# Optimization experiments

Hardware: AMD Instinct MI355X
Metric: run time of the kernel (lower is better)

The kernel has to match this reference:

```python
import jax, jax.numpy as jnp
import numpy as np

B = 32            # batch size
N = 100           # n_nodes (== MAX_N_NODES here)
MAXN = 100        # MAX_N_NODES
H = 256           # HIDDEN_DIM_FEATURES_EXTRACTOR
HA = 1024         # HIDDEN_DIM_ACTOR
HC = 512          # HIDDEN_DIM_CRITIC
K_ACTIVE = 5000   # exact number of active mask entries per batch element


def setup_inputs() -> dict:
    key = jax.random.key(0)
    ks = jax.random.split(key, 16)
    feat = jax.random.normal(ks[0], (B, N + 1, H), jnp.float32)
    # mask: exactly K_ACTIVE ones among N*N per batch row (dim == K for all rows)
    rng = np.random.default_rng(0)
    mask = np.zeros((B, N * N), np.float32)
    for i in range(B):
        mask[i, rng.choice(N * N, size=K_ACTIVE, replace=False)] = 1.0
    mask = jnp.asarray(mask).reshape(B, N, N)
    ext_mask = jnp.concatenate([jnp.zeros((B, 1, N), jnp.float32), mask], axis=1)  # [B, N+1, N]
    embedded_features = jnp.concatenate([feat, ext_mask], axis=2)  # [B, N+1, H+N]

    def lin(k, fi, fo):
        s = 1.0 / np.sqrt(fi)
        return (jax.random.uniform(k, (fi, fo), jnp.float32, -s, s),
                jax.random.uniform(jax.random.fold_in(k, 1), (fo,), jnp.float32, -s, s))

    aW1, ab1 = lin(ks[1], 3 * H, HA)
    aW2, ab2 = lin(ks[2], HA, HA)
    aW3, ab3 = lin(ks[3], HA, 1)
    cW1, cb1 = lin(ks[4], H, HC)
    cW2, cb2 = lin(ks[5], HC, HC)
    cW3, cb3 = lin(ks[6], HC, 1)
    return dict(embedded_features=embedded_features,
                aW1=aW1, ab1=ab1, aW2=aW2, ab2=ab2, aW3=aW3, ab3=ab3,
                cW1=cW1, cb1=cb1, cW2=cW2, cb2=cb2, cW3=cW3, cb3=cb3,
                K=K_ACTIVE)


def reference(embedded_features, aW1, ab1, aW2, ab2, aW3, ab3,
              cW1, cb1, cW2, cb2, cW3, cb3, K):
    # decompose features
    gn = embedded_features[:, :, :H]
    ext_mask = embedded_features[:, :, H:]
    g = gn[:, :1, :]                      # [B,1,H] graph embedding
    nodes = gn[:, 1:, :]                  # [B,N,H] node embeddings
    mask = ext_mask[:, 1:, :].reshape(B, -1)  # [B, N*N]

    # indexes of active pairs (stable top_k -> ascending indices among ones, like nonzero)
    _, idx = jax.lax.top_k(mask, K)       # [B,K] int32
    idx1 = idx // N
    idx2 = idx % N
    n1 = jnp.take_along_axis(nodes, idx1[:, :, None], axis=1)  # [B,K,H]
    n2 = jnp.take_along_axis(nodes, idx2[:, :, None], axis=1)  # [B,K,H]
    pairs = jnp.concatenate([jnp.broadcast_to(g, (B, K, H)), n1, n2], axis=-1)  # [B,K,3H]

    # actor MLP (tanh hidden activations)
    h = jnp.tanh(pairs @ aW1 + ab1)
    h = jnp.tanh(h @ aW2 + ab2)
    logits = h @ aW3 + ab3                # [B,K,1]
    pi = jax.nn.softmax(logits, axis=1)   # softmax over the K gathered pairs

    # scatter back into padded grid
    shaped = jnp.zeros((B, N * N), pi.dtype).at[jnp.arange(B)[:, None], idx].set(pi[..., 0])
    filled = jnp.zeros((B, MAXN, MAXN), pi.dtype).at[:, :N, :N].set(shaped.reshape(B, N, N))
    filled = filled.reshape(B, MAXN * MAXN)

    # critic MLP on graph embedding
    hv = jnp.tanh(g @ cW1 + cb1)
    hv = jnp.tanh(hv @ cW2 + cb2)
    value = hv @ cW3 + cb3                # [B,1,1]
    return filled, value
```

## Files before the change

kernel.cpp:

```cpp
#include <hip/hip_runtime.h>
#include <stdint.h>

#define AS1 __attribute__((address_space(1)))
#define AS3 __attribute__((address_space(3)))

typedef __bf16 bf16x8 __attribute__((ext_vector_type(8)));
typedef float  f32x4  __attribute__((ext_vector_type(4)));
typedef int    i32x8  __attribute__((ext_vector_type(8)));
typedef float  f32x16 __attribute__((ext_vector_type(16)));

__device__ __forceinline__ float tanh_fast(float x){
    float e = __expf(2.0f * x);
    return 1.0f - 2.0f * __builtin_amdgcn_rcpf(e + 1.0f);
}

__device__ __forceinline__ unsigned short f2bf(float f){
    unsigned int u = __float_as_uint(f);
    u = (u + 0x7fffu + ((u >> 16) & 1u)) >> 16;
    return (unsigned short)u;
}

#define B2F(u, lo, hi) { lo = __uint_as_float((u) << 16); hi = __uint_as_float((u) & 0xffff0000u); }

__global__ __launch_bounds__(256) void k_prep(
    const float* __restrict__ ef,  const float* __restrict__ aW1, const float* __restrict__ ab1,
    const float* __restrict__ aW2,
    const float* __restrict__ cW1, const float* __restrict__ cb1,
    const float* __restrict__ cW2, const float* __restrict__ cb2,
    const float* __restrict__ cW3, const float* __restrict__ cb3,
    int* __restrict__ pairs, unsigned short* __restrict__ w1t,
    unsigned char* __restrict__ w2b, float* __restrict__ g1o, float* __restrict__ out,
    int* __restrict__ qctr)
{
    int blk = blockIdx.x;
    int t = threadIdx.x;
    __shared__ int s_base, s_woff[4], s_wc[4];
    __shared__ float gs[256];
    __shared__ float h1[512], h2[512], wred[4];

    if (blk == 0 && t == 0) qctr[0] = 0;

    if (blk < 32){
        int b = blk;
        if (t == 0) s_base = 0;
        __syncthreads();
        int lane = t & 63, w = t >> 6;
        for (int ch = 0; ch < 40; ++ch){
            int pos = ch * 256 + t;
            bool valid = false;
            if (pos < 10000){
                int r = pos / 100, c = pos - (pos / 100) * 100;
                valid = ef[(size_t)b * 35956 + (size_t)(1 + r) * 356 + 256 + c] != 0.0f;
            }
            unsigned long long bal = __ballot(valid);
            if (lane == 0) s_wc[w] = __popcll(bal);
            __syncthreads();
            if (t == 0){
                int r = s_base;
                for (int q = 0; q < 4; ++q){ s_woff[q] = r; r += s_wc[q]; }
                s_base = r;
            }
            __syncthreads();
            if (valid){
                int rank = __popcll(bal & ((1ull << lane) - 1ull));
                int o = s_woff[w] + rank;
                if (o < 5000) pairs[b * 5000 + o] = pos;
            }
            __syncthreads();
        }
    } else if (blk < 288){
        int tid = (blk - 32) * 256 + t;
        int k8 = tid & 31, c = (tid >> 5) & 1023, s = tid >> 15;
        const float* src = aW1 + (size_t)(256 + s * 256 + k8 * 8) * 1024 + c;
        unsigned int* dst = (unsigned int*)(w1t + (size_t)tid * 8);
#pragma unroll
        for (int jj = 0; jj < 4; ++jj){
            unsigned short lo = f2bf(src[(size_t)(2 * jj) * 1024]);
            unsigned short hi = f2bf(src[(size_t)(2 * jj + 1) * 1024]);
            dst[jj] = (unsigned int)lo | ((unsigned int)hi << 16);
        }
    } else if (blk < 416){
        int tid = (blk - 288) * 256 + t;
        int lane = tid & 63, kt = (tid >> 6) & 15, ct = tid >> 10;
        int lh = lane >> 5, n = lane & 31;
        const float* src = aW2 + (size_t)(kt * 64 + lh * 32) * 1024 + ct * 32 + n;
        unsigned int d[4] = {0u, 0u, 0u, 0u};
#pragma unroll
        for (int j = 0; j < 32; ++j){
            float a = src[(size_t)j * 1024] * 128.0f;
            float f = fabsf(a);
            unsigned int m = f < 0.25f ? 0u : f < 0.75f ? 1u : f < 1.25f ? 2u :
                             f < 1.75f ? 3u : f < 2.5f  ? 4u : f < 3.5f  ? 5u :
                             f < 5.0f  ? 6u : 7u;
            unsigned int nib = m | (a < 0.0f ? 8u : 0u);
            d[j >> 3] |= nib << (4 * (j & 7));
        }
        *(uint4*)(w2b + (size_t)(ct * 16 + kt) * 1024 + lane * 16) =
            make_uint4(d[0], d[1], d[2], d[3]);
    } else if (blk < 448){
        int b = blk - 416;
        gs[t] = ef[(size_t)b * 35956 + t];
        __syncthreads();
        float a0 = 0.f, a1 = 0.f, a2 = 0.f, a3 = 0.f;
        for (int i = 0; i < 256; ++i){
            float gi = gs[i];
            const float* row = aW1 + (size_t)i * 1024;
            a0 += gi * row[t];       a1 += gi * row[t + 256];
            a2 += gi * row[t + 512]; a3 += gi * row[t + 768];
        }
        float* o = g1o + (size_t)b * 1024;
        o[t] = a0 + ab1[t];             o[t + 256] = a1 + ab1[t + 256];
        o[t + 512] = a2 + ab1[t + 512]; o[t + 768] = a3 + ab1[t + 768];
    } else {
        int b = blk - 448;
        gs[t] = ef[(size_t)b * 35956 + t];
        __syncthreads();
        for (int o = t; o < 512; o += 256){
            float a = cb1[o];
            for (int i = 0; i < 256; ++i) a += gs[i] * cW1[(size_t)i * 512 + o];
            h1[o] = tanh_fast(a);
        }
        __syncthreads();
        for (int o = t; o < 512; o += 256){
            float a = cb2[o];
            for (int i = 0; i < 512; ++i) a += h1[i] * cW2[(size_t)i * 512 + o];
            h2[o] = tanh_fast(a);
        }
        __syncthreads();
        float p = h2[t] * cW3[t] + h2[t + 256] * cW3[t + 256];
        for (int m = 32; m >= 1; m >>= 1) p += __shfl_xor(p, m);
        if ((t & 63) == 0) wred[t >> 6] = p;
        __syncthreads();
        if (t == 0) out[320000 + b] = wred[0] + wred[1] + wred[2] + wred[3] + cb3[0];
    }
}

__global__ __launch_bounds__(256) void k_p(const float* __restrict__ ef,
        const unsigned short* __restrict__ w1t, unsigned short* __restrict__ P,
        const float* __restrict__ g1){
    __shared__ __align__(16) unsigned short an[112 * 264];
    int blk = blockIdx.x;
    int cb = blk & 15, s = (blk >> 4) & 1, b = blk >> 5;
    int t = threadIdx.x;
    for (int e = t; e < 25600; e += 256){
        int row = e >> 8, col = e & 255;
        an[row * 264 + col] = f2bf(ef[(size_t)b * 35956 + (size_t)(1 + row) * 356 + col]);
    }
    for (int e = t; e < 3168; e += 256) an[26400 + e] = 0;
    __syncthreads();
    int w = t >> 6, lane = t & 63, quad = lane >> 4, n = lane & 15;
    int c = cb * 64 + w * 16 + n;
    f32x4 acc[7];
#pragma unroll
    for (int m = 0; m < 7; ++m){ f32x4 z = {0.f, 0.f, 0.f, 0.f}; acc[m] = z; }
    const bf16x8* wp = (const bf16x8*)(w1t + (size_t)(s * 1024 + c) * 256);
#pragma unroll
    for (int kt = 0; kt < 8; ++kt){
        bf16x8 bfr = wp[kt * 4 + quad];
#pragma unroll
        for (int m = 0; m < 7; ++m){
            const bf16x8* ap = (const bf16x8*)(an + (m * 16 + n) * 264 + kt * 32 + quad * 8);
            acc[m] = __builtin_amdgcn_mfma_f32_16x16x32_bf16(*ap, bfr, acc[m], 0, 0, 0);
        }
    }
    float addv = (s == 0) ? g1[(size_t)b * 1024 + c] : 0.0f;
    size_t base = (size_t)s * 3276800 + (size_t)b * 102400;
#pragma unroll
    for (int m = 0; m < 7; ++m){
        int r0 = m * 16 + quad * 4;
#pragma unroll
        for (int r = 0; r < 4; ++r){
            int row = r0 + r;
            if (row < 100) P[base + (size_t)row * 1024 + c] = f2bf(acc[m][r] + addv);
        }
    }
}

__global__ __launch_bounds__(256, 2) void k_main(
    const int* __restrict__ pairs,
    const unsigned short* __restrict__ P1, const unsigned short* __restrict__ P2,
    const unsigned char* __restrict__ w2b, const float* __restrict__ ab2,
    const float* __restrict__ aW3, float* __restrict__ logits, int* __restrict__ qctr)
{
    __shared__ __align__(16) unsigned char wbuf[2][16384];
    __shared__ int s_tile;
    int t = threadIdx.x, w = t >> 6, lane = t & 63;
    int lrow = lane & 31, lh = lane >> 5;
    int soff = w * 4096 + lane * 16;

    for (;;){
        if (t == 0) s_tile = atomicAdd(qctr, 1);
        __syncthreads();
        int tt = s_tile;
        if (tt >= 1280) break;
        int b = tt / 40, tile = tt - b * 40;

        {
            const unsigned char* s = w2b + soff;
            unsigned char* d = &wbuf[0][0] + soff;
#pragma unroll
            for (int i = 0; i < 4; ++i)
                __builtin_amdgcn_global_load_lds((AS1 void*)(s + i * 1024),
                                                 (AS3 void*)(d + i * 1024), 16, 0, 0);
        }

        int grow = tile * 128 + w * 32 + lrow;
        int pidx = pairs[b * 5000 + (grow < 5000 ? grow : 4999)];
        int i1 = pidx / 100, i2 = pidx - i1 * 100;
        const uint4* pa = (const uint4*)(P1 + (((size_t)(b * 100 + i1)) << 10)) + lh * 4;
        const uint4* pb = (const uint4*)(P2 + (((size_t)(b * 100 + i2)) << 10)) + lh * 4;

        i32x8 af[16];
#pragma unroll
        for (int kt = 0; kt < 16; ++kt){
            uint4 qa[4], qb[4];
#pragma unroll
            for (int j = 0; j < 4; ++j){ qa[j] = pa[kt * 8 + j]; qb[j] = pb[kt * 8 + j]; }
            int u[8];
#pragma unroll
            for (int j = 0; j < 4; ++j){
                float a0, a1, b0, b1;
                B2F(qa[j].x, a0, a1); B2F(qb[j].x, b0, b1);
                float t0 = tanh_fast(a0 + b0), t1 = tanh_fast(a1 + b1);
                B2F(qa[j].y, a0, a1); B2F(qb[j].y, b0, b1);
                float t2 = tanh_fast(a0 + b0), t3 = tanh_fast(a1 + b1);
                int v0 = __builtin_amdgcn_cvt_pk_fp8_f32(t0, t1, 0, false);
                v0 = __builtin_amdgcn_cvt_pk_fp8_f32(t2, t3, v0, true);
                B2F(qa[j].z, a0, a1); B2F(qb[j].z, b0, b1);
                t0 = tanh_fast(a0 + b0); t1 = tanh_fast(a1 + b1);
                B2F(qa[j].w, a0, a1); B2F(qb[j].w, b0, b1);
                t2 = tanh_fast(a0 + b0); t3 = tanh_fast(a1 + b1);
                int v1 = __builtin_amdgcn_cvt_pk_fp8_f32(t0, t1, 0, false);
                v1 = __builtin_amdgcn_cvt_pk_fp8_f32(t2, t3, v1, true);
                u[j * 2] = v0; u[j * 2 + 1] = v1;
            }
            i32x8 f = {u[0], u[1], u[2], u[3], u[4], u[5], u[6], u[7]};
            af[kt] = f;
        }

        float prt[16];
#pragma unroll
        for (int r = 0; r < 16; ++r) prt[r] = 0.f;
        f32x16 acc0, acc1;

        for (int ct = 0; ct < 32; ++ct){
            __syncthreads();
            if (ct < 31){
                const unsigned char* sp = w2b + (size_t)(ct + 1) * 16384 + soff;
                unsigned char* d = &wbuf[(ct + 1) & 1][0] + soff;
#pragma unroll
                for (int i = 0; i < 4; ++i)
                    __builtin_amdgcn_global_load_lds((AS1 void*)(sp + i * 1024),
                                                     (AS3 void*)(d + i * 1024), 16, 0, 0);
            }
#pragma unroll
            for (int r = 0; r < 16; ++r){ acc0[r] = 0.f; acc1[r] = 0.f; }
            const unsigned char* bb = &wbuf[ct & 1][0] + lane * 16;
#pragma unroll
            for (int k2 = 0; k2 < 16; k2 += 2){
                uint4 q0 = *(const uint4*)(bb + k2 * 1024);
                uint4 q1 = *(const uint4*)(bb + (k2 + 1) * 1024);
                i32x8 b0 = {(int)q0.x, (int)q0.y, (int)q0.z, (int)q0.w, 0, 0, 0, 0};
                i32x8 b1 = {(int)q1.x, (int)q1.y, (int)q1.z, (int)q1.w, 0, 0, 0, 0};
                acc0 = __builtin_amdgcn_mfma_scale_f32_32x32x64_f8f6f4(
                           af[k2],     b0, acc0, 0, 4, 0, 0x7F7F7F7F, 0, 0x78787878);
                acc1 = __builtin_amdgcn_mfma_scale_f32_32x32x64_f8f6f4(
                           af[k2 + 1], b1, acc1, 0, 4, 0, 0x7F7F7F7F, 0, 0x78787878);
            }
            int c = ct * 32 + lrow;
            float w3 = aW3[c], bias = ab2[c];
#pragma unroll
            for (int r = 0; r < 16; ++r)
                prt[r] += tanh_fast(acc0[r] + acc1[r] + bias) * w3;
        }

#pragma unroll
        for (int r = 0; r < 16; ++r){
            float v = prt[r];
            v += __shfl_xor(v, 1); v += __shfl_xor(v, 2); v += __shfl_xor(v, 4);
            v += __shfl_xor(v, 8); v += __shfl_xor(v, 16);
            if (lrow == 0){
                int row = (r & 3) + 8 * (r >> 2) + 4 * lh;
                int g = tile * 128 + w * 32 + row;
                if (g < 5000) logits[b * 5000 + g] = v;
            }
        }
    }
}

__global__ void k_soft(const float* __restrict__ logits, const int* __restrict__ pairs,
                       float* __restrict__ out){
    int b = blockIdx.x, t = threadIdx.x;
    __shared__ float red[4];
    __shared__ float bmS, bsS;
    float* ob = out + (size_t)b * 10000;
    for (int j = t; j < 10000; j += 256) ob[j] = 0.0f;
    const float* lg = logits + b * 5000;
    float m = -1e30f;
    for (int j = t; j < 5000; j += 256) m = fmaxf(m, lg[j]);
    for (int s = 32; s >= 1; s >>= 1) m = fmaxf(m, __shfl_xor(m, s));
    if ((t & 63) == 0) red[t >> 6] = m;
    __syncthreads();
    if (t == 0) bmS = fmaxf(fmaxf(red[0], red[1]), fmaxf(red[2], red[3]));
    __syncthreads();
    float mm = bmS;
    float s = 0.f;
    for (int j = t; j < 5000; j += 256) s += __expf(lg[j] - mm);
    for (int k = 32; k >= 1; k >>= 1) s += __shfl_xor(s, k);
    if ((t & 63) == 0) red[t >> 6] = s;
    __syncthreads();
    if (t == 0) bsS = 1.0f / (red[0] + red[1] + red[2] + red[3]);
    __syncthreads();
    float inv = bsS;
    for (int j = t; j < 5000; j += 256){
        int pos = pairs[b * 5000 + j];
        ob[pos] = __expf(lg[j] - mm) * inv;
    }
}

extern "C" void kernel_launch(void* const* d_in, const int* in_sizes, int n_in,
                              void* d_out, int out_size, void* d_ws, size_t ws_size,
                              hipStream_t stream) {
    (void)in_sizes; (void)n_in; (void)out_size; (void)ws_size;
    const float* ef  = (const float*)d_in[0];
    const float* aW1 = (const float*)d_in[1];
    const float* ab1 = (const float*)d_in[2];
    const float* aW2 = (const float*)d_in[3];
    const float* ab2 = (const float*)d_in[4];
    const float* aW3 = (const float*)d_in[5];
    const float* cW1 = (const float*)d_in[7];
    const float* cb1 = (const float*)d_in[8];
    const float* cW2 = (const float*)d_in[9];
    const float* cb2 = (const float*)d_in[10];
    const float* cW3 = (const float*)d_in[11];
    const float* cb3 = (const float*)d_in[12];
    float* out = (float*)d_out;
    char* ws = (char*)d_ws;
    int*   pairs  = (int*)(ws + 0);
    float* logits = (float*)(ws + 640000);
    float* g1     = (float*)(ws + 1280000);
    unsigned short* P1 = (unsigned short*)(ws + 1411072);
    unsigned short* P2 = (unsigned short*)(ws + 7964672);
    unsigned char*  w2b = (unsigned char*)(ws + 14518272);
    unsigned short* w1t = (unsigned short*)(ws + 15566848);
    int*   qctr   = (int*)(ws + 16615424);

    k_prep <<<480,  256, 0, stream>>>(ef, aW1, ab1, aW2, cW1, cb1, cW2, cb2, cW3, cb3,
                                      pairs, w1t, w2b, g1, out, qctr);
    k_p    <<<1024, 256, 0, stream>>>(ef, w1t, P1, g1);
    k_main <<<512,  256, 0, stream>>>(pairs, P1, P2, w2b, ab2, aW3, logits, qctr);
    k_soft <<<32,   256, 0, stream>>>(logits, pairs, out);
}
```

Before: 342.6 us.

## Make k_main waves independent with per-wave weight streaming and work queue

```diff
diff --git a/kernel.cpp b/kernel.cpp
--- a/kernel.cpp
+++ b/kernel.cpp
@@ -182,29 +182,31 @@
     const unsigned char* __restrict__ w2b, const float* __restrict__ ab2,
     const float* __restrict__ aW3, float* __restrict__ logits, int* __restrict__ qctr)
 {
-    __shared__ __align__(16) unsigned char wbuf[2][16384];
-    __shared__ int s_tile;
+    __shared__ __align__(16) unsigned char sbuf[4][2][8192];
+    __shared__ float saw3[1024], sab2[1024];
     int t = threadIdx.x, w = t >> 6, lane = t & 63;
     int lrow = lane & 31, lh = lane >> 5;
-    int soff = w * 4096 + lane * 16;
+
+    for (int i = t; i < 1024; i += 256){ saw3[i] = aW3[i]; sab2[i] = ab2[i]; }
+    __syncthreads();
+
+    unsigned char* buf0 = &sbuf[w][0][0] + lane * 16;
+    unsigned char* buf1 = &sbuf[w][1][0] + lane * 16;
+    const unsigned char* wsrc = w2b + lane * 16;
 
     for (;;){
-        if (t == 0) s_tile = atomicAdd(qctr, 1);
-        __syncthreads();
-        int tt = s_tile;
-        if (tt >= 1280) break;
-        int b = tt / 40, tile = tt - b * 40;
-
-        {
-            const unsigned char* s = w2b + soff;
-            unsigned char* d = &wbuf[0][0] + soff;
-#pragma unroll
-            for (int i = 0; i < 4; ++i)
-                __builtin_amdgcn_global_load_lds((AS1 void*)(s + i * 1024),
-                                                 (AS3 void*)(d + i * 1024), 16, 0, 0);
-        }
-
-        int grow = tile * 128 + w * 32 + lrow;
+        int u = 0;
+        if (lane == 0) u = atomicAdd(qctr, 1);
+        u = __shfl(u, 0);
+        if (u >= 5024) break;
+        int b = u / 157, r0 = (u - b * 157) * 32;
+
+#pragma unroll
+        for (int i = 0; i < 8; ++i)
+            __builtin_amdgcn_global_load_lds((AS1 void*)(wsrc + i * 1024),
+                                             (AS3 void*)(buf0 + i * 1024), 16, 0, 0);
+
+        int grow = r0 + lrow;
         int pidx = pairs[b * 5000 + (grow < 5000 ? grow : 4999)];
         int i1 = pidx / 100, i2 = pidx - i1 * 100;
         const uint4* pa = (const uint4*)(P1 + (((size_t)(b * 100 + i1)) << 10)) + lh * 4;
@@ -216,7 +218,7 @@
             uint4 qa[4], qb[4];
 #pragma unroll
             for (int j = 0; j < 4; ++j){ qa[j] = pa[kt * 8 + j]; qb[j] = pb[kt * 8 + j]; }
-            int u[8];
+            int u8[8];
 #pragma unroll
             for (int j = 0; j < 4; ++j){
                 float a0, a1, b0, b1;
@@ -232,9 +234,9 @@
                 t2 = tanh_fast(a0 + b0); t3 = tanh_fast(a1 + b1);
                 int v1 = __builtin_amdgcn_cvt_pk_fp8_f32(t0, t1, 0, false);
                 v1 = __builtin_amdgcn_cvt_pk_fp8_f32(t2, t3, v1, true);
-                u[j * 2] = v0; u[j * 2 + 1] = v1;
-            }
-            i32x8 f = {u[0], u[1], u[2], u[3], u[4], u[5], u[6], u[7]};
+                u8[j * 2] = v0; u8[j * 2 + 1] = v1;
+            }
+            i32x8 f = {u8[0], u8[1], u8[2], u8[3], u8[4], u8[5], u8[6], u8[7]};
             af[kt] = f;
         }
 
@@ -244,22 +246,18 @@
         f32x16 acc0, acc1;
 
         for (int ct = 0; ct < 32; ++ct){
-            __syncthreads();
-            if (ct < 31){
-                const unsigned char* sp = w2b + (size_t)(ct + 1) * 16384 + soff;
-                unsigned char* d = &wbuf[(ct + 1) & 1][0] + soff;
-#pragma unroll
-                for (int i = 0; i < 4; ++i)
-                    __builtin_amdgcn_global_load_lds((AS1 void*)(sp + i * 1024),
-                                                     (AS3 void*)(d + i * 1024), 16, 0, 0);
-            }
+#pragma unroll
+            for (int i = 0; i < 8; ++i)
+                __builtin_amdgcn_global_load_lds(
+                    (AS1 void*)(wsrc + (size_t)(ct * 2 + 1) * 8192 + i * 1024),
+                    (AS3 void*)(buf1 + i * 1024), 16, 0, 0);
+            asm volatile("s_waitcnt vmcnt(8)" ::: "memory");
 #pragma unroll
             for (int r = 0; r < 16; ++r){ acc0[r] = 0.f; acc1[r] = 0.f; }
-            const unsigned char* bb = &wbuf[ct & 1][0] + lane * 16;
-#pragma unroll
-            for (int k2 = 0; k2 < 16; k2 += 2){
-                uint4 q0 = *(const uint4*)(bb + k2 * 1024);
-                uint4 q1 = *(const uint4*)(bb + (k2 + 1) * 1024);
+#pragma unroll
+            for (int k2 = 0; k2 < 8; k2 += 2){
+                uint4 q0 = *(const uint4*)(buf0 + k2 * 1024);
+                uint4 q1 = *(const uint4*)(buf0 + (k2 + 1) * 1024);
                 i32x8 b0 = {(int)q0.x, (int)q0.y, (int)q0.z, (int)q0.w, 0, 0, 0, 0};
                 i32x8 b1 = {(int)q1.x, (int)q1.y, (int)q1.z, (int)q1.w, 0, 0, 0, 0};
                 acc0 = __builtin_amdgcn_mfma_scale_f32_32x32x64_f8f6f4(
@@ -267,8 +265,29 @@
                 acc1 = __builtin_amdgcn_mfma_scale_f32_32x32x64_f8f6f4(
                            af[k2 + 1], b1, acc1, 0, 4, 0, 0x7F7F7F7F, 0, 0x78787878);
             }
+            if (ct < 31){
+#pragma unroll
+                for (int i = 0; i < 8; ++i)
+                    __builtin_amdgcn_global_load_lds(
+                        (AS1 void*)(wsrc + (size_t)(ct + 1) * 16384 + i * 1024),
+                        (AS3 void*)(buf0 + i * 1024), 16, 0, 0);
+                asm volatile("s_waitcnt vmcnt(8)" ::: "memory");
+            } else {
+                asm volatile("s_waitcnt vmcnt(0)" ::: "memory");
+            }
+#pragma unroll
+            for (int k2 = 0; k2 < 8; k2 += 2){
+                uint4 q0 = *(const uint4*)(buf1 + k2 * 1024);
+                uint4 q1 = *(const uint4*)(buf1 + (k2 + 1) * 1024);
+                i32x8 b0 = {(int)q0.x, (int)q0.y, (int)q0.z, (int)q0.w, 0, 0, 0, 0};
+                i32x8 b1 = {(int)q1.x, (int)q1.y, (int)q1.z, (int)q1.w, 0, 0, 0, 0};
+                acc0 = __builtin_amdgcn_mfma_scale_f32_32x32x64_f8f6f4(
+                           af[8 + k2],     b0, acc0, 0, 4, 0, 0x7F7F7F7F, 0, 0x78787878);
+                acc1 = __builtin_amdgcn_mfma_scale_f32_32x32x64_f8f6f4(
+                           af[8 + k2 + 1], b1, acc1, 0, 4, 0, 0x7F7F7F7F, 0, 0x78787878);
+            }
             int c = ct * 32 + lrow;
-            float w3 = aW3[c], bias = ab2[c];
+            float w3 = saw3[c], bias = sab2[c];
 #pragma unroll
             for (int r = 0; r < 16; ++r)
                 prt[r] += tanh_fast(acc0[r] + acc1[r] + bias) * w3;
@@ -281,7 +300,7 @@
             v += __shfl_xor(v, 8); v += __shfl_xor(v, 16);
             if (lrow == 0){
                 int row = (r & 3) + 8 * (r >> 2) + 4 * lh;
-                int g = tile * 128 + w * 32 + row;
+                int g = r0 + row;
                 if (g < 5000) logits[b * 5000 + g] = v;
             }
         }
```

New measurement: 394.3 us. +15.1%, slower.

## Fuse weight prep and node projection into one stage, double W2 LDS chunk

Applied to the files above, without the earlier changes.

```diff
diff --git a/kernel.cpp b/kernel.cpp
--- a/kernel.cpp
+++ b/kernel.cpp
@@ -22,26 +22,85 @@
 
 #define B2F(u, lo, hi) { lo = __uint_as_float((u) << 16); hi = __uint_as_float((u) & 0xffff0000u); }
 
-__global__ __launch_bounds__(256) void k_prep(
+__global__ __launch_bounds__(256) void k_stage1(
     const float* __restrict__ ef,  const float* __restrict__ aW1, const float* __restrict__ ab1,
     const float* __restrict__ aW2,
     const float* __restrict__ cW1, const float* __restrict__ cb1,
     const float* __restrict__ cW2, const float* __restrict__ cb2,
     const float* __restrict__ cW3, const float* __restrict__ cb3,
-    int* __restrict__ pairs, unsigned short* __restrict__ w1t,
-    unsigned char* __restrict__ w2b, float* __restrict__ g1o, float* __restrict__ out,
-    int* __restrict__ qctr)
+    int* __restrict__ pairs, unsigned char* __restrict__ w2b,
+    unsigned short* __restrict__ P, float* __restrict__ out, int* __restrict__ qctr)
 {
     int blk = blockIdx.x;
     int t = threadIdx.x;
+    __shared__ __align__(16) unsigned short an[112 * 264];
+    __shared__ float gsh[256], gpart[4][64];
     __shared__ int s_base, s_woff[4], s_wc[4];
-    __shared__ float gs[256];
-    __shared__ float h1[512], h2[512], wred[4];
-
-    if (blk == 0 && t == 0) qctr[0] = 0;
-
-    if (blk < 32){
-        int b = blk;
+    __shared__ float gs[256], h1[512], h2[512], wred[4];
+
+    if (blk == 1024 && t == 0) qctr[0] = 0;
+
+    if (blk < 1024){
+        int cb = blk & 15, s = (blk >> 4) & 1, b = blk >> 5;
+        for (int e = t; e < 25600; e += 256){
+            int row = e >> 8, col = e & 255;
+            an[row * 264 + col] = f2bf(ef[(size_t)b * 35956 + (size_t)(1 + row) * 356 + col]);
+        }
+        for (int e = t; e < 3168; e += 256) an[26400 + e] = 0;
+        gsh[t] = ef[(size_t)b * 35956 + t];
+        __syncthreads();
+
+        if (s == 0){
+            int cl = t & 63, q = t >> 6;
+            const float* a1p = aW1 + (size_t)(q * 64) * 1024 + cb * 64 + cl;
+            float p = 0.f;
+            for (int i = 0; i < 64; ++i) p += gsh[q * 64 + i] * a1p[(size_t)i * 1024];
+            gpart[q][cl] = p;
+        }
+        __syncthreads();
+
+        int w = t >> 6, lane = t & 63, quad = lane >> 4, n = lane & 15;
+        int c = cb * 64 + w * 16 + n;
+        bf16x8 bfr[8];
+        const float* wp = aW1 + (size_t)(256 + s * 256 + quad * 8) * 1024 + c;
+#pragma unroll
+        for (int kt = 0; kt < 8; ++kt){
+            unsigned int ww[4];
+#pragma unroll
+            for (int jj = 0; jj < 4; ++jj){
+                unsigned short lo = f2bf(wp[(size_t)(kt * 32 + 2 * jj) * 1024]);
+                unsigned short hi = f2bf(wp[(size_t)(kt * 32 + 2 * jj + 1) * 1024]);
+                ww[jj] = (unsigned int)lo | ((unsigned int)hi << 16);
+            }
+            uint4 pk = make_uint4(ww[0], ww[1], ww[2], ww[3]);
+            bfr[kt] = *(bf16x8*)&pk;
+        }
+        f32x4 acc[7];
+#pragma unroll
+        for (int m = 0; m < 7; ++m){ f32x4 z = {0.f, 0.f, 0.f, 0.f}; acc[m] = z; }
+#pragma unroll
+        for (int kt = 0; kt < 8; ++kt){
+#pragma unroll
+            for (int m = 0; m < 7; ++m){
+                const bf16x8* ap = (const bf16x8*)(an + (m * 16 + n) * 264 + kt * 32 + quad * 8);
+                acc[m] = __builtin_amdgcn_mfma_f32_16x16x32_bf16(*ap, bfr[kt], acc[m], 0, 0, 0);
+            }
+        }
+        int cw = w * 16 + n;
+        float addv = (s == 0)
+            ? (gpart[0][cw] + gpart[1][cw] + gpart[2][cw] + gpart[3][cw] + ab1[c]) : 0.0f;
+        size_t base = (size_t)s * 3276800 + (size_t)b * 102400;
+#pragma unroll
+        for (int m = 0; m < 7; ++m){
+            int r0 = m * 16 + quad * 4;
+#pragma unroll
+            for (int r = 0; r < 4; ++r){
+                int row = r0 + r;
+                if (row < 100) P[base + (size_t)row * 1024 + c] = f2bf(acc[m][r] + addv);
+            }
+        }
+    } else if (blk < 1056){
+        int b = blk - 1024;
         if (t == 0) s_base = 0;
         __syncthreads();
         int lane = t & 63, w = t >> 6;
@@ -68,19 +127,8 @@
             }
             __syncthreads();
         }
-    } else if (blk < 288){
-        int tid = (blk - 32) * 256 + t;
-        int k8 = tid & 31, c = (tid >> 5) & 1023, s = tid >> 15;
-        const float* src = aW1 + (size_t)(256 + s * 256 + k8 * 8) * 1024 + c;
-        unsigned int* dst = (unsigned int*)(w1t + (size_t)tid * 8);
-#pragma unroll
-        for (int jj = 0; jj < 4; ++jj){
-            unsigned short lo = f2bf(src[(size_t)(2 * jj) * 1024]);
-            unsigned short hi = f2bf(src[(size_t)(2 * jj + 1) * 1024]);
-            dst[jj] = (unsigned int)lo | ((unsigned int)hi << 16);
-        }
-    } else if (blk < 416){
-        int tid = (blk - 288) * 256 + t;
+    } else if (blk < 1184){
+        int tid = (blk - 1056) * 256 + t;
         int lane = tid & 63, kt = (tid >> 6) & 15, ct = tid >> 10;
         int lh = lane >> 5, n = lane & 31;
         const float* src = aW2 + (size_t)(kt * 64 + lh * 32) * 1024 + ct * 32 + n;
@@ -97,22 +145,8 @@
         }
         *(uint4*)(w2b + (size_t)(ct * 16 + kt) * 1024 + lane * 16) =
             make_uint4(d[0], d[1], d[2], d[3]);
-    } else if (blk < 448){
-        int b = blk - 416;
-        gs[t] = ef[(size_t)b * 35956 + t];
-        __syncthreads();
-        float a0 = 0.f, a1 = 0.f, a2 = 0.f, a3 = 0.f;
-        for (int i = 0; i < 256; ++i){
-            float gi = gs[i];
-            const float* row = aW1 + (size_t)i * 1024;
-            a0 += gi * row[t];       a1 += gi * row[t + 256];
-            a2 += gi * row[t + 512]; a3 += gi * row[t + 768];
-        }
-        float* o = g1o + (size_t)b * 1024;
-        o[t] = a0 + ab1[t];             o[t + 256] = a1 + ab1[t + 256];
-        o[t + 512] = a2 + ab1[t + 512]; o[t + 768] = a3 + ab1[t + 768];
     } else {
-        int b = blk - 448;
+        int b = blk - 1184;
         gs[t] = ef[(size_t)b * 35956 + t];
         __syncthreads();
         for (int o = t; o < 512; o += 256){
@@ -132,47 +166,6 @@
         if ((t & 63) == 0) wred[t >> 6] = p;
         __syncthreads();
         if (t == 0) out[320000 + b] = wred[0] + wred[1] + wred[2] + wred[3] + cb3[0];
-    }
-}
-
-__global__ __launch_bounds__(256) void k_p(const float* __restrict__ ef,
-        const unsigned short* __restrict__ w1t, unsigned short* __restrict__ P,
-        const float* __restrict__ g1){
-    __shared__ __align__(16) unsigned short an[112 * 264];
-    int blk = blockIdx.x;
-    int cb = blk & 15, s = (blk >> 4) & 1, b = blk >> 5;
-    int t = threadIdx.x;
-    for (int e = t; e < 25600; e += 256){
-        int row = e >> 8, col = e & 255;
-        an[row * 264 + col] = f2bf(ef[(size_t)b * 35956 + (size_t)(1 + row) * 356 + col]);
-    }
-    for (int e = t; e < 3168; e += 256) an[26400 + e] = 0;
-    __syncthreads();
-    int w = t >> 6, lane = t & 63, quad = lane >> 4, n = lane & 15;
-    int c = cb * 64 + w * 16 + n;
-    f32x4 acc[7];
-#pragma unroll
-    for (int m = 0; m < 7; ++m){ f32x4 z = {0.f, 0.f, 0.f, 0.f}; acc[m] = z; }
-    const bf16x8* wp = (const bf16x8*)(w1t + (size_t)(s * 1024 + c) * 256);
-#pragma unroll
-    for (int kt = 0; kt < 8; ++kt){
-        bf16x8 bfr = wp[kt * 4 + quad];
-#pragma unroll
-        for (int m = 0; m < 7; ++m){
-            const bf16x8* ap = (const bf16x8*)(an + (m * 16 + n) * 264 + kt * 32 + quad * 8);
-            acc[m] = __builtin_amdgcn_mfma_f32_16x16x32_bf16(*ap, bfr, acc[m], 0, 0, 0);
-        }
-    }
-    float addv = (s == 0) ? g1[(size_t)b * 1024 + c] : 0.0f;
-    size_t base = (size_t)s * 3276800 + (size_t)b * 102400;
-#pragma unroll
-    for (int m = 0; m < 7; ++m){
-        int r0 = m * 16 + quad * 4;
-#pragma unroll
-        for (int r = 0; r < 4; ++r){
-            int row = r0 + r;
-            if (row < 100) P[base + (size_t)row * 1024 + c] = f2bf(acc[m][r] + addv);
-        }
     }
 }
 
@@ -182,11 +175,14 @@
     const unsigned char* __restrict__ w2b, const float* __restrict__ ab2,
     const float* __restrict__ aW3, float* __restrict__ logits, int* __restrict__ qctr)
 {
-    __shared__ __align__(16) unsigned char wbuf[2][16384];
+    __shared__ __align__(16) unsigned char wbuf[2][32768];
+    __shared__ float saw3[1024], sab2[1024];
     __shared__ int s_tile;
     int t = threadIdx.x, w = t >> 6, lane = t & 63;
     int lrow = lane & 31, lh = lane >> 5;
-    int soff = w * 4096 + lane * 16;
+    int soff = w * 8192 + lane * 16;
+
+    for (int i = t; i < 1024; i += 256){ saw3[i] = aW3[i]; sab2[i] = ab2[i]; }
 
     for (;;){
         if (t == 0) s_tile = atomicAdd(qctr, 1);
@@ -199,7 +195,7 @@
             const unsigned char* s = w2b + soff;
             unsigned char* d = &wbuf[0][0] + soff;
 #pragma unroll
-            for (int i = 0; i < 4; ++i)
+            for (int i = 0; i < 8; ++i)
                 __builtin_amdgcn_global_load_lds((AS1 void*)(s + i * 1024),
                                                  (AS3 void*)(d + i * 1024), 16, 0, 0);
         }
@@ -216,7 +212,7 @@
             uint4 qa[4], qb[4];
 #pragma unroll
             for (int j = 0; j < 4; ++j){ qa[j] = pa[kt * 8 + j]; qb[j] = pb[kt * 8 + j]; }
-            int u[8];
+            int u8[8];
 #pragma unroll
             for (int j = 0; j < 4; ++j){
                 float a0, a1, b0, b1;
@@ -232,9 +228,9 @@
                 t2 = tanh_fast(a0 + b0); t3 = tanh_fast(a1 + b1);
                 int v1 = __builtin_amdgcn_cvt_pk_fp8_f32(t0, t1, 0, false);
                 v1 = __builtin_amdgcn_cvt_pk_fp8_f32(t2, t3, v1, true);
-                u[j * 2] = v0; u[j * 2 + 1] = v1;
-            }
-            i32x8 f = {u[0], u[1], u[2], u[3], u[4], u[5], u[6], u[7]};
+                u8[j * 2] = v0; u8[j * 2 + 1] = v1;
+            }
+            i32x8 f = {u8[0], u8[1], u8[2], u8[3], u8[4], u8[5], u8[6], u8[7]};
             af[kt] = f;
         }
 
@@ -243,35 +239,39 @@
         for (int r = 0; r < 16; ++r) prt[r] = 0.f;
         f32x16 acc0, acc1;
 
-        for (int ct = 0; ct < 32; ++ct){
+        for (int cp = 0; cp < 16; ++cp){
             __syncthreads();
-            if (ct < 31){
-                const unsigned char* sp = w2b + (size_t)(ct + 1) * 16384 + soff;
-                unsigned char* d = &wbuf[(ct + 1) & 1][0] + soff;
-#pragma unroll
-                for (int i = 0; i < 4; ++i)
+            if (cp < 15){
+                const unsigned char* sp = w2b + (size_t)(cp + 1) * 32768 + soff;
+                unsigned char* d = &wbuf[(cp + 1) & 1][0] + soff;
+#pragma unroll
+                for (int i = 0; i < 8; ++i)
                     __builtin_amdgcn_global_load_lds((AS1 void*)(sp + i * 1024),
                                                      (AS3 void*)(d + i * 1024), 16, 0, 0);
             }
 #pragma unroll
-            for (int r = 0; r < 16; ++r){ acc0[r] = 0.f; acc1[r] = 0.f; }
-            const unsigned char* bb = &wbuf[ct & 1][0] + lane * 16;
-#pragma unroll
-            for (int k2 = 0; k2 < 16; k2 += 2){
-                uint4 q0 = *(const uint4*)(bb + k2 * 1024);
-                uint4 q1 = *(const uint4*)(bb + (k2 + 1) * 1024);
-                i32x8 b0 = {(int)q0.x, (int)q0.y, (int)q0.z, (int)q0.w, 0, 0, 0, 0};
-                i32x8 b1 = {(int)q1.x, (int)q1.y, (int)q1.z, (int)q1.w, 0, 0, 0, 0};
-                acc0 = __builtin_amdgcn_mfma_scale_f32_32x32x64_f8f6f4(
-                           af[k2],     b0, acc0, 0, 4, 0, 0x7F7F7F7F, 0, 0x78787878);
-                acc1 = __builtin_amdgcn_mfma_scale_f32_32x32x64_f8f6f4(
-                           af[k2 + 1], b1, acc1, 0, 4, 0, 0x7F7F7F7F, 0, 0x78787878);
-            }
-            int c = ct * 32 + lrow;
-            float w3 = aW3[c], bias = ab2[c];
-#pragma unroll
-            for (int r = 0; r < 16; ++r)
-                prt[r] += tanh_fast(acc0[r] + acc1[r] + bias) * w3;
+            for (int half = 0; half < 2; ++half){
+                int ct = cp * 2 + half;
+                const unsigned char* bb = &wbuf[cp & 1][0] + half * 16384 + lane * 16;
+#pragma unroll
+                for (int r = 0; r < 16; ++r){ acc0[r] = 0.f; acc1[r] = 0.f; }
+#pragma unroll
+                for (int k2 = 0; k2 < 16; k2 += 2){
+                    uint4 q0 = *(const uint4*)(bb + k2 * 1024);
+                    uint4 q1 = *(const uint4*)(bb + (k2 + 1) * 1024);
+                    i32x8 b0 = {(int)q0.x, (int)q0.y, (int)q0.z, (int)q0.w, 0, 0, 0, 0};
+                    i32x8 b1 = {(int)q1.x, (int)q1.y, (int)q1.z, (int)q1.w, 0, 0, 0, 0};
+                    acc0 = __builtin_amdgcn_mfma_scale_f32_32x32x64_f8f6f4(
+                               af[k2],     b0, acc0, 0, 4, 0, 0x7F7F7F7F, 0, 0x78787878);
+                    acc1 = __builtin_amdgcn_mfma_scale_f32_32x32x64_f8f6f4(
+                               af[k2 + 1], b1, acc1, 0, 4, 0, 0x7F7F7F7F, 0, 0x78787878);
+                }
+                int c = ct * 32 + lrow;
+                float w3 = saw3[c], bias = sab2[c];
+#pragma unroll
+                for (int r = 0; r < 16; ++r)
+                    prt[r] += tanh_fast(acc0[r] + acc1[r] + bias) * w3;
+            }
         }
 
 #pragma unroll
@@ -338,16 +338,13 @@
     char* ws = (char*)d_ws;
     int*   pairs  = (int*)(ws + 0);
     float* logits = (float*)(ws + 640000);
-    float* g1     = (float*)(ws + 1280000);
     unsigned short* P1 = (unsigned short*)(ws + 1411072);
     unsigned short* P2 = (unsigned short*)(ws + 7964672);
     unsigned char*  w2b = (unsigned char*)(ws + 14518272);
-    unsigned short* w1t = (unsigned short*)(ws + 15566848);
     int*   qctr   = (int*)(ws + 16615424);
 
-    k_prep <<<480,  256, 0, stream>>>(ef, aW1, ab1, aW2, cW1, cb1, cW2, cb2, cW3, cb3,
-                                      pairs, w1t, w2b, g1, out, qctr);
-    k_p    <<<1024, 256, 0, stream>>>(ef, w1t, P1, g1);
-    k_main <<<512,  256, 0, stream>>>(pairs, P1, P2, w2b, ab2, aW3, logits, qctr);
-    k_soft <<<32,   256, 0, stream>>>(logits, pairs, out);
-}
+    k_stage1<<<1216, 256, 0, stream>>>(ef, aW1, ab1, aW2, cW1, cb1, cW2, cb2, cW3, cb3,
+                                       pairs, w2b, P1, out, qctr);
+    k_main  <<<512,  256, 0, stream>>>(pairs, P1, P2, w2b, ab2, aW3, logits, qctr);
+    k_soft  <<<32,   256, 0, stream>>>(logits, pairs, out);
+}
```

New measurement: 343.7 us. Within noise of the previous version (+0.3%).
